# Performance work log

Hardware: AMD Instinct MI355X
Metric: run time of the kernel (lower is better)

## Reference

```python
import jax, jax.numpy as jnp
import numpy as np

DIM = 768
NUM_HEADS = 12
HEAD_DIM = DIM // NUM_HEADS
SCALE = HEAD_DIM ** -0.5


def setup_inputs() -> dict:
    key = jax.random.key(0)
    k_x, k_m, k_qkv, k_proj, k_b = jax.random.split(key, 5)
    B, N, C = 4, 2048, DIM
    x = jax.random.normal(k_x, (B, N, C), dtype=jnp.float32)
    # boolean mask [N, N]; True = masked position (masked_fill semantics)
    mask = jax.random.randint(k_m, (N, N), 0, 2).astype(jnp.bool_)
    # qkv Linear(dim, 3*dim, bias=False): store as [C, 3C] for x @ W
    w_qkv = jax.random.normal(k_qkv, (C, 3 * C), dtype=jnp.float32) * (C ** -0.5)
    # proj Linear(dim, dim) with bias
    w_proj = jax.random.normal(k_proj, (C, C), dtype=jnp.float32) * (C ** -0.5)
    b_proj = jax.random.normal(k_b, (C,), dtype=jnp.float32) * 0.02
    return {"x": x, "mask": mask, "w_qkv": w_qkv, "w_proj": w_proj, "b_proj": b_proj}


def reference(x, mask, w_qkv, w_proj, b_proj):
    B, N, C = x.shape
    H, D = NUM_HEADS, HEAD_DIM
    qkv = (x @ w_qkv).reshape(B, N, 3, H, D)
    q = qkv[:, :, 0].transpose(0, 2, 1, 3)  # [B, H, N, D]
    k = qkv[:, :, 1].transpose(0, 2, 1, 3)
    v = qkv[:, :, 2].transpose(0, 2, 1, 3)
    attn = jnp.einsum("bhnd,bhmd->bhnm", q, k) * SCALE  # [B, H, N, N]
    attn = jnp.where(mask[None, None, :, :], -jnp.inf, attn)
    attn = jax.nn.softmax(attn, axis=-1)
    # dropout p=0.0 (eval) -> identity
    out = jnp.einsum("bhnm,bhmd->bhnd", attn, v)  # [B, H, N, D]
    out = out.transpose(0, 2, 1, 3).reshape(B, N, C)
    return out @ w_proj + b_proj
```

## Files before the change

### kernel.cpp

```cpp
#include <hip/hip_runtime.h>

#define NSEQ 2048
#define CDIM 768
#define NBATCH 4
#define NHEAD 12
#define HD 64
#define MTOT (NBATCH * NSEQ)
#define NQKV (3 * CDIM)

typedef float f32x4 __attribute__((ext_vector_type(4)));
typedef short bf16x8 __attribute__((ext_vector_type(8)));
typedef short short4v __attribute__((ext_vector_type(4)));

__device__ __forceinline__ short f2bf(float f) {
  union { float f; unsigned u; } x; x.f = f;
  unsigned r = x.u + 0x7fffu + ((x.u >> 16) & 1u);
  return (short)(r >> 16);
}

__device__ __forceinline__ void gload16(const short* g, short* l) {
  __builtin_amdgcn_global_load_lds((const __attribute__((address_space(1))) void*)g,
                                   (__attribute__((address_space(3))) void*)l, 16, 0, 0);
}

__device__ __forceinline__ const bf16x8* frag(const short* t, int row, int col) {
  int byt = (row << 7) + (col << 1);
  byt ^= (row & 7) << 4;
  return (const bf16x8*)((const char*)t + byt);
}

__global__ __launch_bounds__(256) void detect_mask(const unsigned char* __restrict__ m,
                                                   int* __restrict__ flag) {
  __shared__ int f1, f23;
  if (threadIdx.x == 0) { f1 = 0; f23 = 0; }
  __syncthreads();
  int a = 0, b = 0;
  for (int i = threadIdx.x; i < 1024; i += 256) {
    if (m[i * 4 + 1]) a = 1;
    if (m[i * 4 + 2] | m[i * 4 + 3]) b = 1;
  }
  if (a) atomicOr(&f1, 1);
  if (b) atomicOr(&f23, 1);
  __syncthreads();
  if (threadIdx.x == 0) *flag = f1 ? 1 : (f23 ? 2 : 0);
}

__global__ __launch_bounds__(256) void pack_mask(const void* __restrict__ mask,
                                                 const int* __restrict__ flag,
                                                 unsigned* __restrict__ bits) {
  int wi = blockIdx.x * 256 + threadIdx.x;
  int f = *flag;
  unsigned v = 0;
  if (f == 1) {
    const unsigned char* p = (const unsigned char*)mask + (size_t)wi * 32;
#pragma unroll
    for (int j = 0; j < 32; ++j) v |= (p[j] != 0 ? 1u : 0u) << j;
  } else if (f == 2) {
    const float* p = (const float*)mask + (size_t)wi * 32;
#pragma unroll
    for (int j = 0; j < 32; ++j) v |= (p[j] != 0.f ? 1u : 0u) << j;
  } else {
    const int* p = (const int*)mask + (size_t)wi * 32;
#pragma unroll
    for (int j = 0; j < 32; ++j) v |= (p[j] != 0 ? 1u : 0u) << j;
  }
  bits[wi] = v;
}

__global__ __launch_bounds__(256) void conv_bf16(const float* __restrict__ in,
                                                 short* __restrict__ out, int n) {
  int i = (blockIdx.x * 256 + threadIdx.x) * 8;
  if (i >= n) return;
  f32x4 a = *(const f32x4*)&in[i];
  f32x4 b = *(const f32x4*)&in[i + 4];
  bf16x8 o;
#pragma unroll
  for (int j = 0; j < 4; ++j) o[j] = f2bf(a[j]);
#pragma unroll
  for (int j = 0; j < 4; ++j) o[4 + j] = f2bf(b[j]);
  *(bf16x8*)&out[i] = o;
}

__global__ __launch_bounds__(256) void transpose_conv(const float* __restrict__ in,
                                                      short* __restrict__ outp,
                                                      int R, int Cc) {
  __shared__ short tile[64][65];
  int c0 = blockIdx.x * 64, r0 = blockIdx.y * 64;
  int t = threadIdx.x;
  int tr = t >> 4;
  int tc = (t & 15) * 4;
  for (int rr = tr; rr < 64; rr += 16) {
    f32x4 v = *(const f32x4*)&in[(size_t)(r0 + rr) * Cc + c0 + tc];
#pragma unroll
    for (int j = 0; j < 4; ++j) tile[tc + j][rr] = f2bf(v[j]);
  }
  __syncthreads();
  for (int cc = tr; cc < 64; cc += 16) {
#pragma unroll
    for (int j = 0; j < 4; ++j)
      outp[(size_t)(c0 + cc) * R + r0 + tc + j] = tile[cc][tc + j];
  }
}

__global__ __launch_bounds__(256) void vtrans(const short* __restrict__ qkvb,
                                              short* __restrict__ vt) {
  __shared__ short t[64][72];
  int n0 = blockIdx.x * 64, bh = blockIdx.y;
  int b = bh / NHEAD, h = bh % NHEAD;
  int tid = threadIdx.x, r = tid >> 2, c0 = (tid & 3) * 16;
  const short* src = qkvb + (size_t)(b * NSEQ + n0 + r) * NQKV + 2 * CDIM + h * HD + c0;
  bf16x8 v0 = *(const bf16x8*)src;
  bf16x8 v1 = *(const bf16x8*)(src + 8);
  *(bf16x8*)&t[r][c0] = v0;
  *(bf16x8*)&t[r][c0 + 8] = v1;
  __syncthreads();
  bf16x8 o0, o1;
#pragma unroll
  for (int j = 0; j < 8; ++j) { o0[j] = t[c0 + j][r]; o1[j] = t[c0 + 8 + j][r]; }
  short* dst = vt + (size_t)(bh * HD + r) * NSEQ + n0 + c0;
  *(bf16x8*)&dst[0] = o0;
  *(bf16x8*)&dst[8] = o1;
}

template <bool F32OUT>
__global__ __launch_bounds__(256) void gemm_bt(const short* __restrict__ A,
                                               const short* __restrict__ Bt,
                                               void* __restrict__ Cout,
                                               const float* __restrict__ bias,
                                               int Mdim, int Ndim, int Kdim) {
  __shared__ short As[128 * 32];
  __shared__ short Bs[128 * 32];
  const int tid = threadIdx.x;
  const int lane = tid & 63;
  const int w = tid >> 6;
  const int wm = (w >> 1) * 64, wn = (w & 1) * 64;
  const int lr = lane & 15, lh = lane >> 4;
  const int m0 = blockIdx.y * 128, n0 = blockIdx.x * 128;

  f32x4 acc[4][4];
#pragma unroll
  for (int i = 0; i < 4; ++i)
#pragma unroll
    for (int j = 0; j < 4; ++j) acc[i][j] = (f32x4){0.f, 0.f, 0.f, 0.f};

  const int srow = w * 32 + (lane >> 2);
  const int scol = (lane & 3) * 8;
  const short* Ap = A + (size_t)(m0 + srow) * Kdim + scol;
  const short* Bp = Bt + (size_t)(n0 + srow) * Kdim + scol;
  short* AsW0 = &As[(w * 32) * 32];
  short* AsW1 = &As[(w * 32 + 16) * 32];
  short* BsW0 = &Bs[(w * 32) * 32];
  short* BsW1 = &Bs[(w * 32 + 16) * 32];

  for (int k0 = 0; k0 < Kdim; k0 += 32) {
    __syncthreads();
    gload16(Ap + k0, AsW0);
    gload16(Ap + (size_t)16 * Kdim + k0, AsW1);
    gload16(Bp + k0, BsW0);
    gload16(Bp + (size_t)16 * Kdim + k0, BsW1);
    __syncthreads();
    bf16x8 a[4], b[4];
#pragma unroll
    for (int i = 0; i < 4; ++i) a[i] = *(const bf16x8*)&As[(wm + i * 16 + lr) * 32 + lh * 8];
#pragma unroll
    for (int j = 0; j < 4; ++j) b[j] = *(const bf16x8*)&Bs[(wn + j * 16 + lr) * 32 + lh * 8];
#pragma unroll
    for (int i = 0; i < 4; ++i)
#pragma unroll
      for (int j = 0; j < 4; ++j)
        acc[i][j] = __builtin_amdgcn_mfma_f32_16x16x32_bf16(a[i], b[j], acc[i][j], 0, 0, 0);
  }

#pragma unroll
  for (int i = 0; i < 4; ++i) {
    int mrowb = m0 + wm + i * 16 + lh * 4;
#pragma unroll
    for (int j = 0; j < 4; ++j) {
      int ncol = n0 + wn + j * 16 + lr;
#pragma unroll
      for (int r = 0; r < 4; ++r) {
        float v = acc[i][j][r];
        if (F32OUT)
          ((float*)Cout)[(size_t)(mrowb + r) * Ndim + ncol] = v + bias[ncol];
        else
          ((short*)Cout)[(size_t)(mrowb + r) * Ndim + ncol] = f2bf(v);
      }
    }
  }
}

__global__ __launch_bounds__(256) void flash_attn(const short* __restrict__ qkv,
                                                  const short* __restrict__ vtb,
                                                  const unsigned long long* __restrict__ mbits,
                                                  short* __restrict__ outp) {
  __shared__ short Qs[64 * 64];
  __shared__ short Ks[64 * 64];
  __shared__ short Vt[64 * 64];

  const int tid = threadIdx.x;
  const int lane = tid & 63;
  const int w = tid >> 6;
  const int lr = lane & 15, lh = lane >> 4;
  const int q0 = blockIdx.x * 64;
  const int bh = blockIdx.y;
  const int b = bh / NHEAD, h = bh % NHEAD;

  const int srow = lane >> 3;
  const int schunk = (lane & 7) ^ srow;

  {
    const short* qb = qkv + (size_t)(b * NSEQ + q0 + w * 16 + srow) * NQKV + h * HD + schunk * 8;
    gload16(qb, &Qs[(w * 16) * 64]);
    gload16(qb + (size_t)8 * NQKV, &Qs[(w * 16 + 8) * 64]);
  }
  __syncthreads();
  const bf16x8 qf0 = *frag(Qs, w * 16 + lr, lh * 8);
  const bf16x8 qf1 = *frag(Qs, w * 16 + lr, 32 + lh * 8);

  float m_r = -1e30f, l_r = 0.f;
  f32x4 o[4];
#pragma unroll
  for (int nd = 0; nd < 4; ++nd) o[nd] = (f32x4){0.f, 0.f, 0.f, 0.f};

  const short* kbase = qkv + (size_t)(b * NSEQ) * NQKV + CDIM + h * HD;
  const short* vbase = vtb + (size_t)(bh * HD) * NSEQ;
  const int srcA = (lh & 1) * 32 + lr;
  const int srcB = srcA + 16;
  const int nbh = lh >> 1;

  for (int kv0 = 0; kv0 < NSEQ; kv0 += 64) {
    unsigned long long mw = mbits[(size_t)(q0 + w * 16 + lr) * (NSEQ / 64) + (kv0 >> 6)];
    __syncthreads();
    {
      const short* kb = kbase + (size_t)(kv0 + w * 16 + srow) * NQKV + schunk * 8;
      gload16(kb, &Ks[(w * 16) * 64]);
      gload16(kb + (size_t)8 * NQKV, &Ks[(w * 16 + 8) * 64]);
      const short* vb = vbase + (size_t)(w * 16 + srow) * NSEQ + kv0 + schunk * 8;
      gload16(vb, &Vt[(w * 16) * 64]);
      gload16(vb + (size_t)8 * NSEQ, &Vt[(w * 16 + 8) * 64]);
    }
    __syncthreads();

    float p[4][4];
#pragma unroll
    for (int nb = 0; nb < 4; ++nb) {
      f32x4 st = (f32x4){0.f, 0.f, 0.f, 0.f};
      st = __builtin_amdgcn_mfma_f32_16x16x32_bf16(*frag(Ks, nb * 16 + lr, lh * 8), qf0, st, 0, 0, 0);
      st = __builtin_amdgcn_mfma_f32_16x16x32_bf16(*frag(Ks, nb * 16 + lr, 32 + lh * 8), qf1, st, 0, 0, 0);
      unsigned m4 = ((unsigned)(mw >> (nb * 16 + lh * 4))) & 15u;
#pragma unroll
      for (int r = 0; r < 4; ++r)
        p[nb][r] = ((m4 >> r) & 1u) ? -3e38f : st[r] * 0.125f;
    }

    float pm = p[0][0];
#pragma unroll
    for (int nb = 0; nb < 4; ++nb)
#pragma unroll
      for (int r = 0; r < 4; ++r) pm = fmaxf(pm, p[nb][r]);
    pm = fmaxf(pm, __shfl_xor(pm, 16, 64));
    pm = fmaxf(pm, __shfl_xor(pm, 32, 64));
    float nm = fmaxf(m_r, pm);
    float al = __expf(m_r - nm);
    m_r = nm;
    float rs = 0.f;
#pragma unroll
    for (int nb = 0; nb < 4; ++nb)
#pragma unroll
      for (int r = 0; r < 4; ++r) {
        float e = __expf(p[nb][r] - nm);
        p[nb][r] = e;
        rs += e;
      }
    rs += __shfl_xor(rs, 16, 64);
    rs += __shfl_xor(rs, 32, 64);
    l_r = l_r * al + rs;
#pragma unroll
    for (int nd = 0; nd < 4; ++nd)
#pragma unroll
      for (int r = 0; r < 4; ++r) o[nd][r] *= al;

    unsigned pk[4][2];
#pragma unroll
    for (int nb = 0; nb < 4; ++nb) {
      asm("v_cvt_pk_bf16_f32 %0, %1, %2" : "=v"(pk[nb][0]) : "v"(p[nb][0]), "v"(p[nb][1]));
      asm("v_cvt_pk_bf16_f32 %0, %1, %2" : "=v"(pk[nb][1]) : "v"(p[nb][2]), "v"(p[nb][3]));
    }
    bf16x8 pb[2];
#pragma unroll
    for (int c = 0; c < 2; ++c) {
      unsigned a0 = __shfl(pk[2 * c][0], srcA, 64);
      unsigned a1 = __shfl(pk[2 * c][1], srcA, 64);
      unsigned a2 = __shfl(pk[2 * c][0], srcB, 64);
      unsigned a3 = __shfl(pk[2 * c][1], srcB, 64);
      unsigned b0 = __shfl(pk[2 * c + 1][0], srcA, 64);
      unsigned b1 = __shfl(pk[2 * c + 1][1], srcA, 64);
      unsigned b2 = __shfl(pk[2 * c + 1][0], srcB, 64);
      unsigned b3 = __shfl(pk[2 * c + 1][1], srcB, 64);
      union { unsigned u[4]; bf16x8 v; } uu;
      uu.u[0] = nbh ? b0 : a0;
      uu.u[1] = nbh ? b1 : a1;
      uu.u[2] = nbh ? b2 : a2;
      uu.u[3] = nbh ? b3 : a3;
      pb[c] = uu.v;
    }

#pragma unroll
    for (int nd = 0; nd < 4; ++nd) {
      o[nd] = __builtin_amdgcn_mfma_f32_16x16x32_bf16(*frag(Vt, nd * 16 + lr, lh * 8), pb[0], o[nd], 0, 0, 0);
      o[nd] = __builtin_amdgcn_mfma_f32_16x16x32_bf16(*frag(Vt, nd * 16 + lr, 32 + lh * 8), pb[1], o[nd], 0, 0, 0);
    }
  }

  const float inv = 1.f / l_r;
  short* orow = outp + (size_t)(b * NSEQ + q0 + w * 16 + lr) * CDIM + h * HD + lh * 4;
#pragma unroll
  for (int nd = 0; nd < 4; ++nd) {
    short4v sv;
#pragma unroll
    for (int r = 0; r < 4; ++r) sv[r] = f2bf(o[nd][r] * inv);
    *(short4v*)&orow[nd * 16] = sv;
  }
}

extern "C" void kernel_launch(void* const* d_in, const int* in_sizes, int n_in,
                              void* d_out, int out_size, void* d_ws, size_t ws_size,
                              hipStream_t stream) {
  const float* x      = (const float*)d_in[0];
  const void*  mask   = d_in[1];
  const float* w_qkv  = (const float*)d_in[2];
  const float* w_proj = (const float*)d_in[3];
  const float* b_proj = (const float*)d_in[4];
  float* outp = (float*)d_out;
  char* ws = (char*)d_ws;

  int*      flag   = (int*)(ws + 0);
  unsigned* mbits  = (unsigned*)(ws + 1024);
  short*    xb     = (short*)(ws + 525312);
  short*    wqkvT  = (short*)(ws + 25691136);
  short*    wprojT = (short*)(ws + 29230080);
  short*    qkvb   = (short*)(ws + 30409728);
  short*    attnb  = (short*)(ws + 68158464);
  short*    vtb    = xb;

  detect_mask<<<1, 256, 0, stream>>>((const unsigned char*)mask, flag);
  pack_mask<<<512, 256, 0, stream>>>(mask, flag, mbits);
  conv_bf16<<<(MTOT * CDIM) / 2048, 256, 0, stream>>>(x, xb, MTOT * CDIM);
  transpose_conv<<<dim3(NQKV / 64, CDIM / 64), 256, 0, stream>>>(w_qkv, wqkvT, CDIM, NQKV);
  transpose_conv<<<dim3(CDIM / 64, CDIM / 64), 256, 0, stream>>>(w_proj, wprojT, CDIM, CDIM);
  gemm_bt<false><<<dim3(NQKV / 128, MTOT / 128), 256, 0, stream>>>(xb, wqkvT, qkvb, nullptr,
                                                                   MTOT, NQKV, CDIM);
  vtrans<<<dim3(NSEQ / 64, NBATCH * NHEAD), 256, 0, stream>>>(qkvb, vtb);
  flash_attn<<<dim3(NSEQ / 64, NBATCH * NHEAD), 256, 0, stream>>>(
      qkvb, vtb, (const unsigned long long*)mbits, attnb);
  gemm_bt<true><<<dim3(CDIM / 128, MTOT / 128), 256, 0, stream>>>(attnb, wprojT, outp, b_proj,
                                                                  MTOT, CDIM, CDIM);
}
```

Measured before the change: 313.6 us.

## Double-buffer LDS tiles in GEMM and flash attention, add lazy softmax rescale

Both the projection GEMM and the flash-attention kernel now double-buffer their LDS tiles. The next K/V (or A/B) tile is issued with global_load_lds before computing the current one, and vmcnt waits with raw barriers replace the paired __syncthreads. The attention kernel also loads Q fragments directly from global memory instead of staging them through LDS, and prefetches the mask word. The softmax switches to a base-2 exponent via v_exp_f32 with the scale folded into log2e, and rescales the running max and accumulators only when the new max exceeds the old by more than 8. Together these aim to hide memory latency and cut exp and rescale ALU work, at the cost of more LDS, reliance on manual vmcnt counting, and looser bounds on intermediate values.

Measured after the change: 308.9 us. About the same (-1.5%).

```diff
diff --git a/kernel.cpp b/kernel.cpp
--- a/kernel.cpp
+++ b/kernel.cpp
@@ -16,6 +16,10 @@
   union { float f; unsigned u; } x; x.f = f;
   unsigned r = x.u + 0x7fffu + ((x.u >> 16) & 1u);
   return (short)(r >> 16);
+}
+
+__device__ __forceinline__ float exp2a(float x) {
+  float r; asm("v_exp_f32 %0, %1" : "=v"(r) : "v"(x)); return r;
 }
 
 __device__ __forceinline__ void gload16(const short* g, short* l) {
@@ -128,8 +132,8 @@
                                                void* __restrict__ Cout,
                                                const float* __restrict__ bias,
                                                int Mdim, int Ndim, int Kdim) {
-  __shared__ short As[128 * 32];
-  __shared__ short Bs[128 * 32];
+  __shared__ short As[2][128 * 32];
+  __shared__ short Bs[2][128 * 32];
   const int tid = threadIdx.x;
   const int lane = tid & 63;
   const int w = tid >> 6;
@@ -147,29 +151,43 @@
   const int scol = (lane & 3) * 8;
   const short* Ap = A + (size_t)(m0 + srow) * Kdim + scol;
   const short* Bp = Bt + (size_t)(n0 + srow) * Kdim + scol;
-  short* AsW0 = &As[(w * 32) * 32];
-  short* AsW1 = &As[(w * 32 + 16) * 32];
-  short* BsW0 = &Bs[(w * 32) * 32];
-  short* BsW1 = &Bs[(w * 32 + 16) * 32];
-
-  for (int k0 = 0; k0 < Kdim; k0 += 32) {
-    __syncthreads();
-    gload16(Ap + k0, AsW0);
-    gload16(Ap + (size_t)16 * Kdim + k0, AsW1);
-    gload16(Bp + k0, BsW0);
-    gload16(Bp + (size_t)16 * Kdim + k0, BsW1);
-    __syncthreads();
+  const int l0 = (w * 32) * 32;
+  const int l1 = (w * 32 + 16) * 32;
+
+  auto tilecompute = [&](const short* Asb, const short* Bsb) {
     bf16x8 a[4], b[4];
 #pragma unroll
-    for (int i = 0; i < 4; ++i) a[i] = *(const bf16x8*)&As[(wm + i * 16 + lr) * 32 + lh * 8];
-#pragma unroll
-    for (int j = 0; j < 4; ++j) b[j] = *(const bf16x8*)&Bs[(wn + j * 16 + lr) * 32 + lh * 8];
+    for (int i = 0; i < 4; ++i) a[i] = *(const bf16x8*)&Asb[(wm + i * 16 + lr) * 32 + lh * 8];
+#pragma unroll
+    for (int j = 0; j < 4; ++j) b[j] = *(const bf16x8*)&Bsb[(wn + j * 16 + lr) * 32 + lh * 8];
 #pragma unroll
     for (int i = 0; i < 4; ++i)
 #pragma unroll
       for (int j = 0; j < 4; ++j)
         acc[i][j] = __builtin_amdgcn_mfma_f32_16x16x32_bf16(a[i], b[j], acc[i][j], 0, 0, 0);
-  }
+  };
+
+  gload16(Ap, &As[0][l0]);
+  gload16(Ap + (size_t)16 * Kdim, &As[0][l1]);
+  gload16(Bp, &Bs[0][l0]);
+  gload16(Bp + (size_t)16 * Kdim, &Bs[0][l1]);
+
+  const int NT = Kdim >> 5;
+  for (int t = 0; t < NT - 1; ++t) {
+    const int cur = t & 1, nxt = cur ^ 1;
+    const int k1 = (t + 1) << 5;
+    gload16(Ap + k1, &As[nxt][l0]);
+    gload16(Ap + (size_t)16 * Kdim + k1, &As[nxt][l1]);
+    gload16(Bp + k1, &Bs[nxt][l0]);
+    gload16(Bp + (size_t)16 * Kdim + k1, &Bs[nxt][l1]);
+    asm volatile("s_waitcnt vmcnt(4)" ::: "memory");
+    __builtin_amdgcn_s_barrier();
+    tilecompute(As[cur], Bs[cur]);
+    __builtin_amdgcn_s_barrier();
+  }
+  asm volatile("s_waitcnt vmcnt(0)" ::: "memory");
+  __builtin_amdgcn_s_barrier();
+  tilecompute(As[(NT - 1) & 1], Bs[(NT - 1) & 1]);
 
 #pragma unroll
   for (int i = 0; i < 4; ++i) {
@@ -193,9 +211,8 @@
                                                   const short* __restrict__ vtb,
                                                   const unsigned long long* __restrict__ mbits,
                                                   short* __restrict__ outp) {
-  __shared__ short Qs[64 * 64];
-  __shared__ short Ks[64 * 64];
-  __shared__ short Vt[64 * 64];
+  __shared__ short KB[2][64 * 64];
+  __shared__ short VB[2][64 * 64];
 
   const int tid = threadIdx.x;
   const int lane = tid & 63;
@@ -208,49 +225,43 @@
   const int srow = lane >> 3;
   const int schunk = (lane & 7) ^ srow;
 
-  {
-    const short* qb = qkv + (size_t)(b * NSEQ + q0 + w * 16 + srow) * NQKV + h * HD + schunk * 8;
-    gload16(qb, &Qs[(w * 16) * 64]);
-    gload16(qb + (size_t)8 * NQKV, &Qs[(w * 16 + 8) * 64]);
-  }
-  __syncthreads();
-  const bf16x8 qf0 = *frag(Qs, w * 16 + lr, lh * 8);
-  const bf16x8 qf1 = *frag(Qs, w * 16 + lr, 32 + lh * 8);
+  const short* qrow = qkv + (size_t)(b * NSEQ + q0 + w * 16 + lr) * NQKV + h * HD;
+  const bf16x8 qf0 = *(const bf16x8*)(qrow + lh * 8);
+  const bf16x8 qf1 = *(const bf16x8*)(qrow + 32 + lh * 8);
+  asm volatile("" ::: "memory");
+
+  const short* kbase = qkv + (size_t)(b * NSEQ + w * 16 + srow) * NQKV + CDIM + h * HD + schunk * 8;
+  const short* vbase = vtb + (size_t)(bh * HD + w * 16 + srow) * NSEQ + schunk * 8;
+
+  gload16(kbase, &KB[0][(w * 16) * 64]);
+  gload16(kbase + (size_t)8 * NQKV, &KB[0][(w * 16 + 8) * 64]);
+  gload16(vbase, &VB[0][(w * 16) * 64]);
+  gload16(vbase + (size_t)8 * NSEQ, &VB[0][(w * 16 + 8) * 64]);
+
+  const unsigned long long* mrow = mbits + (size_t)(q0 + w * 16 + lr) * (NSEQ / 64);
+  unsigned long long mw = mrow[0];
 
   float m_r = -1e30f, l_r = 0.f;
   f32x4 o[4];
 #pragma unroll
   for (int nd = 0; nd < 4; ++nd) o[nd] = (f32x4){0.f, 0.f, 0.f, 0.f};
 
-  const short* kbase = qkv + (size_t)(b * NSEQ) * NQKV + CDIM + h * HD;
-  const short* vbase = vtb + (size_t)(bh * HD) * NSEQ;
   const int srcA = (lh & 1) * 32 + lr;
   const int srcB = srcA + 16;
   const int nbh = lh >> 1;
-
-  for (int kv0 = 0; kv0 < NSEQ; kv0 += 64) {
-    unsigned long long mw = mbits[(size_t)(q0 + w * 16 + lr) * (NSEQ / 64) + (kv0 >> 6)];
-    __syncthreads();
-    {
-      const short* kb = kbase + (size_t)(kv0 + w * 16 + srow) * NQKV + schunk * 8;
-      gload16(kb, &Ks[(w * 16) * 64]);
-      gload16(kb + (size_t)8 * NQKV, &Ks[(w * 16 + 8) * 64]);
-      const short* vb = vbase + (size_t)(w * 16 + srow) * NSEQ + kv0 + schunk * 8;
-      gload16(vb, &Vt[(w * 16) * 64]);
-      gload16(vb + (size_t)8 * NSEQ, &Vt[(w * 16 + 8) * 64]);
-    }
-    __syncthreads();
-
+  const float C2 = 0.18033688f;
+
+  auto compute = [&](const short* Kb, const short* Vb, unsigned long long mwv) {
     float p[4][4];
 #pragma unroll
     for (int nb = 0; nb < 4; ++nb) {
       f32x4 st = (f32x4){0.f, 0.f, 0.f, 0.f};
-      st = __builtin_amdgcn_mfma_f32_16x16x32_bf16(*frag(Ks, nb * 16 + lr, lh * 8), qf0, st, 0, 0, 0);
-      st = __builtin_amdgcn_mfma_f32_16x16x32_bf16(*frag(Ks, nb * 16 + lr, 32 + lh * 8), qf1, st, 0, 0, 0);
-      unsigned m4 = ((unsigned)(mw >> (nb * 16 + lh * 4))) & 15u;
+      st = __builtin_amdgcn_mfma_f32_16x16x32_bf16(*frag(Kb, nb * 16 + lr, lh * 8), qf0, st, 0, 0, 0);
+      st = __builtin_amdgcn_mfma_f32_16x16x32_bf16(*frag(Kb, nb * 16 + lr, 32 + lh * 8), qf1, st, 0, 0, 0);
+      unsigned m4 = ((unsigned)(mwv >> (nb * 16 + lh * 4))) & 15u;
 #pragma unroll
       for (int r = 0; r < 4; ++r)
-        p[nb][r] = ((m4 >> r) & 1u) ? -3e38f : st[r] * 0.125f;
+        p[nb][r] = ((m4 >> r) & 1u) ? -3e38f : st[r] * C2;
     }
 
     float pm = p[0][0];
@@ -260,25 +271,29 @@
       for (int r = 0; r < 4; ++r) pm = fmaxf(pm, p[nb][r]);
     pm = fmaxf(pm, __shfl_xor(pm, 16, 64));
     pm = fmaxf(pm, __shfl_xor(pm, 32, 64));
-    float nm = fmaxf(m_r, pm);
-    float al = __expf(m_r - nm);
-    m_r = nm;
+
+    if (__any(pm > m_r + 8.f)) {
+      float nm = fmaxf(m_r, pm);
+      float al = exp2a(m_r - nm);
+      m_r = nm;
+      l_r *= al;
+#pragma unroll
+      for (int nd = 0; nd < 4; ++nd)
+#pragma unroll
+        for (int r = 0; r < 4; ++r) o[nd][r] *= al;
+    }
     float rs = 0.f;
 #pragma unroll
     for (int nb = 0; nb < 4; ++nb)
 #pragma unroll
       for (int r = 0; r < 4; ++r) {
-        float e = __expf(p[nb][r] - nm);
+        float e = exp2a(p[nb][r] - m_r);
         p[nb][r] = e;
         rs += e;
       }
     rs += __shfl_xor(rs, 16, 64);
     rs += __shfl_xor(rs, 32, 64);
-    l_r = l_r * al + rs;
-#pragma unroll
-    for (int nd = 0; nd < 4; ++nd)
-#pragma unroll
-      for (int r = 0; r < 4; ++r) o[nd][r] *= al;
+    l_r += rs;
 
     unsigned pk[4][2];
 #pragma unroll
@@ -307,10 +322,31 @@
 
 #pragma unroll
     for (int nd = 0; nd < 4; ++nd) {
-      o[nd] = __builtin_amdgcn_mfma_f32_16x16x32_bf16(*frag(Vt, nd * 16 + lr, lh * 8), pb[0], o[nd], 0, 0, 0);
-      o[nd] = __builtin_amdgcn_mfma_f32_16x16x32_bf16(*frag(Vt, nd * 16 + lr, 32 + lh * 8), pb[1], o[nd], 0, 0, 0);
-    }
-  }
+      o[nd] = __builtin_amdgcn_mfma_f32_16x16x32_bf16(*frag(Vb, nd * 16 + lr, lh * 8), pb[0], o[nd], 0, 0, 0);
+      o[nd] = __builtin_amdgcn_mfma_f32_16x16x32_bf16(*frag(Vb, nd * 16 + lr, 32 + lh * 8), pb[1], o[nd], 0, 0, 0);
+    }
+  };
+
+  for (int t = 0; t < 31; ++t) {
+    const int cur = t & 1, nxt = cur ^ 1;
+    {
+      const short* kb = kbase + (size_t)(t + 1) * 64 * NQKV;
+      gload16(kb, &KB[nxt][(w * 16) * 64]);
+      gload16(kb + (size_t)8 * NQKV, &KB[nxt][(w * 16 + 8) * 64]);
+      const short* vb = vbase + (t + 1) * 64;
+      gload16(vb, &VB[nxt][(w * 16) * 64]);
+      gload16(vb + (size_t)8 * NSEQ, &VB[nxt][(w * 16 + 8) * 64]);
+    }
+    asm volatile("s_waitcnt vmcnt(4)" ::: "memory");
+    unsigned long long mw_next = mrow[t + 1];
+    __builtin_amdgcn_s_barrier();
+    compute(KB[cur], VB[cur], mw);
+    mw = mw_next;
+    __builtin_amdgcn_s_barrier();
+  }
+  asm volatile("s_waitcnt vmcnt(0)" ::: "memory");
+  __builtin_amdgcn_s_barrier();
+  compute(KB[1], VB[1], mw);
 
   const float inv = 1.f / l_r;
   short* orow = outp + (size_t)(b * NSEQ + q0 + w * 16 + lr) * CDIM + h * HD + lh * 4;
```
